# Kernel tuning notes

Measured on AMD Instinct MI355X. Metric: run time of the kernel, lower is better.

The kernel has to match this reference:

```python
import jax, jax.numpy as jnp
import numpy as np

B, F, M, D = 1024, 4, 512, 8192  # batch, factors, codebook size, hypervector dim
ITERS = 10


def _sign(x):
    # bipolar quantize: >=0 -> +1, <0 -> -1 (MAP VSA 'multiset quantize' / sign)
    return jnp.where(x >= 0, 1.0, -1.0).astype(x.dtype)


def setup_inputs() -> dict:
    key = jax.random.key(0)
    k1, k2 = jax.random.split(key, 2)
    # bipolar codebooks: (F, M, D)
    codebooks = _sign(jax.random.normal(k1, (F, M, D), dtype=jnp.float32))
    # composite input: bind (elementwise product) of one random codevector per factor
    idx = jax.random.randint(k2, (B, F), 0, M)  # ground-truth factor indices
    chosen = codebooks[jnp.arange(F)[None, :], idx]  # (B, F, D)
    inp = jnp.prod(chosen, axis=1)  # (B, D), bipolar
    # init estimates = quantized multiset (superposition) of each codebook, per the
    # module's get_init_estimates, broadcast over batch
    init_est = jnp.broadcast_to(_sign(codebooks.sum(axis=1))[None], (B, F, D))
    init_est = jnp.asarray(init_est, dtype=jnp.float32)
    return {"input": inp, "init_estimates": init_est, "codebooks": codebooks}


def reference(input, init_estimates, codebooks):
    """CONCURRENT resonator, SOFTWARE (bipolar MAP) mode, activation='NONE'.

    Returns (outcome indices (B,F) int32, convergence iteration k, final estimates).
    """

    def stage(est):
        # For bipolar +/-1 vectors: multibind(all other factors) = prod(all) * est
        prod_all = jnp.prod(est, axis=1)                      # (B, D)
        new_est = input[:, None, :] * prod_all[:, None, :] * est  # (B, F, D)
        sim = jnp.einsum('bfd,fmd->bfm', new_est, codebooks)  # dot_similarity
        out = _sign(jnp.einsum('bfm,fmd->bfd', sim, codebooks))  # multiset, quantize
        return out, sim.max(axis=-1)

    def step(carry, _):
        est, k, done = carry
        new_est, _max_sim = stage(est)
        conv = jnp.all(new_est == est)  # old_estimates == estimates check
        k = k + jnp.where(done, 0, 1)
        done = done | conv
        return (new_est, k, done), None

    init = (init_estimates, jnp.array(0, jnp.int32), jnp.array(False))
    (est, k, _done), _ = jax.lax.scan(step, init, None, length=ITERS)

    # cleanup: argmax of |dot_similarity| per factor (argmax_abs=True)
    sim = jnp.einsum('bfd,fmd->bfm', est, codebooks)
    outcome = jnp.argmax(jnp.abs(sim), axis=-1).astype(jnp.int32)  # (B, F)
    return outcome, k, est
```

## Files before the change

### kernel.cpp

```cpp
#include <hip/hip_runtime.h>
#include <stdint.h>

#define B_ 1024
#define F_ 4
#define M_ 512
#define D_ 8192
#define ITERS_ 10
#define DW_ 128
#define SMSZ2 32768

typedef unsigned long long u64;
typedef unsigned int u32;
typedef unsigned short u16;
typedef signed char i8;

typedef int i32x4 __attribute__((ext_vector_type(4)));
typedef u64 u64x2 __attribute__((ext_vector_type(2)));

struct Flags { u32 done; u32 k; u32 conv[ITERS_]; };

__device__ inline void gload_lds16(const void* g, void* l){
  __builtin_amdgcn_global_load_lds(
      (const __attribute__((address_space(1))) void*)g,
      (__attribute__((address_space(3))) void*)l, 16, 0, 0);
}

__device__ inline bool conv_prefix_done(const u32* conv, int iter){
  bool d = false;
  for (int j = 0; j < iter; ++j) d |= (conv[j] != 0u);
  return d;
}

__global__ void k_bitify(const float* __restrict__ src, u64* __restrict__ dst){
  long gid = (long)blockIdx.x * 256 + threadIdx.x;
  float v = src[gid];
  u64 m = __ballot(v < 0.0f);
  if ((threadIdx.x & 63) == 0) dst[gid >> 6] = m;
}

__global__ void k_bitify0(const float* __restrict__ init_est, u64* __restrict__ tmp0,
                          Flags* fl){
  long gid = (long)blockIdx.x * 256 + threadIdx.x;
  float v = init_est[gid];
  u64 m = __ballot(v < 0.0f);
  if ((threadIdx.x & 63) == 0) tmp0[gid >> 6] = m;
  if (blockIdx.x == 0){
    if (threadIdx.x == 0){ fl->done = 0; fl->k = 0; }
    if (threadIdx.x < ITERS_) fl->conv[threadIdx.x] = 1u;
  }
}

__global__ void k_bcast(const u64* __restrict__ tmp0, u64* __restrict__ estbits){
  long gid = (long)blockIdx.x * 256 + threadIdx.x;
  estbits[gid] = tmp0[gid & (F_*DW_ - 1)];
}

__global__ void k_cb_prep(const float* __restrict__ cb, u64* __restrict__ cbbT,
                          i8* __restrict__ cbT8){
  __shared__ i8 tile[64][68];
  int bx = blockIdx.x;
  int f = bx >> 10;
  int r = bx & 1023;
  int mt = r >> 7, dt = r & 127;
  for (int it = 0; it < 16; ++it){
    int lid = threadIdx.x + it*256;
    int i = lid >> 6, j = lid & 63;
    float v = cb[((long)(f*M_ + mt*64 + i))*D_ + dt*64 + j];
    tile[j][i] = (v < 0.0f) ? (i8)-1 : (i8)1;
    u64 msk = __ballot(v < 0.0f);
    if (j == 0) cbbT[((long)(f*DW_ + dt))*M_ + mt*64 + i] = msk;
  }
  __syncthreads();
  for (int it = 0; it < 4; ++it){
    int lid = threadIdx.x + it*256;
    int dd = lid >> 4, mg = lid & 15;
    u32 p = (u32)(unsigned char)tile[dd][mg*4+0]
          | ((u32)(unsigned char)tile[dd][mg*4+1] << 8)
          | ((u32)(unsigned char)tile[dd][mg*4+2] << 16)
          | ((u32)(unsigned char)tile[dd][mg*4+3] << 24);
    *(u32*)(cbT8 + ((long)(f*D_ + dt*64 + dd))*M_ + mt*64 + mg*4) = p;
  }
}

__global__ __launch_bounds__(256) void k_forward2(
    const u64* __restrict__ inbits, const u64* __restrict__ estbits,
    const u64* __restrict__ cbbT, i8* __restrict__ Aq, i8* __restrict__ Ar,
    const Flags* __restrict__ fl, int iter){
  if (conv_prefix_done(fl->conv, iter)) return;
  __shared__ u64 nbs[DW_][10];
  int id = blockIdx.x;
  int rr = id & 7;
  int f   = rr & 3;
  int btl = rr >> 2;
  int q   = id >> 3;
  int bth = q & 63;
  int mh  = q >> 6;
  int bt  = bth*2 + btl;
  int b0  = bt * 8;
  int tid = threadIdx.x;
  for (int idx = tid; idx < 8*DW_; idx += 256){
    int w = idx & 127, bb = idx >> 7;
    const u64* eb = estbits + (long)(b0 + bb)*F_*DW_;
    u64 all = eb[w] ^ eb[DW_+w] ^ eb[2*DW_+w] ^ eb[3*DW_+w];
    nbs[w][bb] = inbits[(long)(b0 + bb)*DW_ + w] ^ all ^ eb[f*DW_ + w];
  }
  __syncthreads();
  int m = mh*256 + tid;
  int acc[8];
  #pragma unroll
  for (int bb = 0; bb < 8; ++bb) acc[bb] = 0;
  const u64* cbf = cbbT + (long)f*DW_*M_ + m;
  #pragma unroll 2
  for (int w = 0; w < DW_; ++w){
    u64 c = cbf[(long)w*M_];
    u64x2 n01 = *(const u64x2*)&nbs[w][0];
    u64x2 n23 = *(const u64x2*)&nbs[w][2];
    u64x2 n45 = *(const u64x2*)&nbs[w][4];
    u64x2 n67 = *(const u64x2*)&nbs[w][6];
    acc[0] += (int)__popcll(n01.x ^ c);
    acc[1] += (int)__popcll(n01.y ^ c);
    acc[2] += (int)__popcll(n23.x ^ c);
    acc[3] += (int)__popcll(n23.y ^ c);
    acc[4] += (int)__popcll(n45.x ^ c);
    acc[5] += (int)__popcll(n45.y ^ c);
    acc[6] += (int)__popcll(n67.x ^ c);
    acc[7] += (int)__popcll(n67.y ^ c);
  }
  #pragma unroll
  for (int bb = 0; bb < 8; ++bb){
    int v = 4096 - acc[bb];
    int r = ((v + 32) & 63) - 32;
    int qd = (v - r) >> 6;
    long base = ((long)(f*B_ + b0 + bb))*M_ + m;
    Aq[base] = (i8)qd;
    Ar[base] = (i8)r;
  }
}

__global__ __launch_bounds__(256, 2) void k_backward_d256(
    const i8* __restrict__ Aq, const i8* __restrict__ Ar, const i8* __restrict__ cbT8,
    u64* __restrict__ estbits, Flags* fl, int iter){
  if (conv_prefix_done(fl->conv, iter)) return;
  __shared__ __attribute__((aligned(16))) i8 smem[2*SMSZ2];
  int id = blockIdx.x;
  int rr = id & 7;
  int f  = rr >> 1;
  int dh = rr & 1;
  int qq = id >> 3;
  int bt = qq & 7;
  int dtl= qq >> 3;
  int dtp= dh*16 + dtl;
  int b0 = bt*128, d0 = dtp*256;
  int tid = threadIdx.x;
  int wv = tid >> 6, lane = tid & 63, l16 = lane & 15, quad = lane >> 4;
  int rl = lane >> 2, pl = lane & 3;

  i32x4 zero = {0, 0, 0, 0};
  i32x4 acc[2][16];
  #pragma unroll
  for (int i = 0; i < 2; ++i)
    #pragma unroll
    for (int j = 0; j < 16; ++j) acc[i][j] = zero;

  const i8* Aqg = Aq + ((long)f*B_ + b0)*M_;
  const i8* Arg = Ar + ((long)f*B_ + b0)*M_;
  const i8* Bg  = cbT8 + ((long)f*D_ + d0)*M_;

  const i8* gsrc[8];
  i8* lbase[8];
  int swz = (rl >> 1) & 3;
  #pragma unroll
  for (int j2 = 0; j2 < 8; ++j2){
    int job = j2*4 + wv;
    const i8* src; i8* lb; int jj;
    if (job < 8)      { src = Aqg; jj = job;      lb = smem +         jj*1024; }
    else if (job < 16){ src = Arg; jj = job - 8;  lb = smem +  8192 + jj*1024; }
    else              { src = Bg;  jj = job - 16; lb = smem + 16384 + jj*1024; }
    gsrc[j2]  = src + (long)(jj*16 + rl)*M_ + ((pl ^ swz) << 4);
    lbase[j2] = lb;
  }

  #pragma unroll
  for (int j2 = 0; j2 < 8; ++j2)
    gload_lds16(gsrc[j2], lbase[j2]);

  for (int kt = 0; kt < 8; ++kt){
    __syncthreads();
    if (kt < 7){
      int nb = (kt + 1) & 1, k0 = (kt + 1)*64;
      #pragma unroll
      for (int j2 = 0; j2 < 8; ++j2)
        gload_lds16(gsrc[j2] + k0, lbase[j2] + nb*SMSZ2);
    }
    const i8* sb = smem + (kt & 1)*SMSZ2;
    i32x4 aq[2], ar[2];
    #pragma unroll
    for (int rt = 0; rt < 2; ++rt){
      int row = wv*32 + rt*16 + l16;
      int c = (quad ^ ((row >> 1) & 3)) << 4;
      aq[rt] = *(const i32x4*)(sb +        row*64 + c);
      ar[rt] = *(const i32x4*)(sb + 8192 + row*64 + c);
    }
    #pragma unroll
    for (int ct = 0; ct < 16; ++ct){
      int rowB = ct*16 + l16;
      int c = (quad ^ ((rowB >> 1) & 3)) << 4;
      i32x4 bb = *(const i32x4*)(sb + 16384 + rowB*64 + c);
      i32x4 bb64;
      #pragma unroll
      for (int g = 0; g < 4; ++g)
        bb64[g] = (int)(((u32)bb[g] << 6) & 0xC0C0C0C0u);
      acc[0][ct] = __builtin_amdgcn_mfma_i32_16x16x64_i8(aq[0], bb64, acc[0][ct], 0, 0, 0);
      acc[0][ct] = __builtin_amdgcn_mfma_i32_16x16x64_i8(ar[0], bb,   acc[0][ct], 0, 0, 0);
      acc[1][ct] = __builtin_amdgcn_mfma_i32_16x16x64_i8(aq[1], bb64, acc[1][ct], 0, 0, 0);
      acc[1][ct] = __builtin_amdgcn_mfma_i32_16x16x64_i8(ar[1], bb,   acc[1][ct], 0, 0, 0);
    }
  }

  int q3 = (lane >> 2) & 3, pw = lane & 3;
  int pw1 = pw & 1, pw2 = pw >> 1;
  u64 wreg[2][4];
  #pragma unroll
  for (int rt = 0; rt < 2; ++rt){
    #pragma unroll
    for (int r = 0; r < 4; ++r){
      u64 g0[4], g1[4], g2[4], g3[4];
      #pragma unroll
      for (int c = 0; c < 4; ++c){
        g0[c] = __ballot(acc[rt][c][r]      < 0);
        g1[c] = __ballot(acc[rt][4 + c][r]  < 0);
        g2[c] = __ballot(acc[rt][8 + c][r]  < 0);
        g3[c] = __ballot(acc[rt][12 + c][r] < 0);
      }
      u64 word = 0;
      #pragma unroll
      for (int c = 0; c < 4; ++c){
        u64 s = pw2 ? (pw1 ? g3[c] : g2[c]) : (pw1 ? g1[c] : g0[c]);
        word |= ((s >> (16*q3)) & 0xFFFFull) << (16*c);
      }
      wreg[rt][r] = word;
    }
  }
  u64 oldv[2][4];
  if (lane < 16){
    #pragma unroll
    for (int rt = 0; rt < 2; ++rt)
      #pragma unroll
      for (int r = 0; r < 4; ++r){
        int row = wv*32 + rt*16 + q3*4 + r;
        oldv[rt][r] = estbits[((long)(b0 + row)*F_ + f)*DW_ + dtp*4 + pw];
      }
  }
  u32 flag = 0;
  if (lane < 16){
    #pragma unroll
    for (int rt = 0; rt < 2; ++rt)
      #pragma unroll
      for (int r = 0; r < 4; ++r){
        int row = wv*32 + rt*16 + q3*4 + r;
        long addr = ((long)(b0 + row)*F_ + f)*DW_ + dtp*4 + pw;
        estbits[addr] = wreg[rt][r];
        flag |= (oldv[rt][r] != wreg[rt][r]) ? 1u : 0u;
      }
  }
  u32 mymiss = (u32)(__ballot(flag != 0) != 0ull);
  if (lane == 0 && mymiss) atomicAnd(&fl->conv[iter], 0u);
}

__global__ __launch_bounds__(256) void k_outcome(
    const u64* __restrict__ estbits, const u64* __restrict__ cbbT,
    const Flags* __restrict__ fl, float* __restrict__ out){
  __shared__ u64 es[8][DW_];
  __shared__ int redv[4][8], redi[4][8];
  int f = blockIdx.y, b0 = blockIdx.x * 8;
  int tid = threadIdx.x, wv = tid >> 6, lane = tid & 63;
  for (int idx = tid; idx < 8*DW_; idx += 256){
    int bb = idx >> 7, w = idx & 127;
    es[bb][w] = estbits[((long)(b0 + bb)*F_ + f)*DW_ + w];
  }
  __syncthreads();
  const u64* cbf = cbbT + (long)f*DW_*M_;
  int m0 = tid, m1 = tid + 256;
  int acc0[8], acc1[8];
  #pragma unroll
  for (int bb = 0; bb < 8; ++bb){ acc0[bb] = 0; acc1[bb] = 0; }
  for (int w = 0; w < DW_; ++w){
    u64 c0 = cbf[(long)w*M_ + m0];
    u64 c1 = cbf[(long)w*M_ + m1];
    #pragma unroll
    for (int bb = 0; bb < 8; ++bb){
      u64 e = es[bb][w];
      acc0[bb] += (int)__popcll(e ^ c0);
      acc1[bb] += (int)__popcll(e ^ c1);
    }
  }
  int bv[8], bi[8];
  #pragma unroll
  for (int bb = 0; bb < 8; ++bb){
    int a0 = 4096 - acc0[bb]; if (a0 < 0) a0 = -a0;
    int a1 = 4096 - acc1[bb]; if (a1 < 0) a1 = -a1;
    bv[bb] = a0; bi[bb] = m0;
    if (a1 > a0){ bv[bb] = a1; bi[bb] = m1; }
  }
  for (int off = 32; off; off >>= 1){
    #pragma unroll
    for (int bb = 0; bb < 8; ++bb){
      int ov = __shfl_xor(bv[bb], off, 64);
      int oi = __shfl_xor(bi[bb], off, 64);
      if (ov > bv[bb] || (ov == bv[bb] && oi < bi[bb])){ bv[bb] = ov; bi[bb] = oi; }
    }
  }
  if (lane == 0)
    #pragma unroll
    for (int bb = 0; bb < 8; ++bb){ redv[wv][bb] = bv[bb]; redi[wv][bb] = bi[bb]; }
  __syncthreads();
  if (tid < 8){
    int v0 = redv[0][tid], i0 = redi[0][tid];
    for (int w = 1; w < 4; ++w){
      int v = redv[w][tid], i = redi[w][tid];
      if (v > v0 || (v == v0 && i < i0)){ v0 = v; i0 = i; }
    }
    out[(long)(b0 + tid)*F_ + f] = (float)i0;
  }
  if (blockIdx.x == 0 && f == 0 && tid == 0){
    int k = ITERS_;
    for (int j = 0; j < ITERS_; ++j) if (fl->conv[j]){ k = j + 1; break; }
    out[B_*F_] = (float)k;
  }
}

__global__ void k_unpack(const u64* __restrict__ estbits, float* __restrict__ out){
  long gid = (long)blockIdx.x*256 + threadIdx.x;
  int bf = (int)(gid >> 11);
  int d4 = (int)(gid & 2047);
  u64 word = estbits[(long)bf*DW_ + (d4 >> 4)];
  u32 nib = (u32)(word >> ((d4 & 15) * 4)) & 0xFu;
  long base = (long)(B_*F_ + 1) + (long)bf*D_ + (long)d4*4;
  out[base+0] = (nib & 1u) ? -1.0f : 1.0f;
  out[base+1] = (nib & 2u) ? -1.0f : 1.0f;
  out[base+2] = (nib & 4u) ? -1.0f : 1.0f;
  out[base+3] = (nib & 8u) ? -1.0f : 1.0f;
}

extern "C" void kernel_launch(void* const* d_in, const int* in_sizes, int n_in,
                              void* d_out, int out_size, void* d_ws, size_t ws_size,
                              hipStream_t stream){
  const float* input    = (const float*)d_in[0];
  const float* init_est = (const float*)d_in[1];
  const float* cb       = (const float*)d_in[2];
  char* ws   = (char*)d_ws;
  char* outc = (char*)d_out;

  size_t off = 0;
  Flags* fl = (Flags*)(ws); off = 1024;
  u64* tmp0    = (u64*)(ws + off); off += (size_t)F_*DW_*8;
  off = (off + 1023) & ~size_t(1023);
  u64* inbits  = (u64*)(ws + off); off += (size_t)B_*DW_*8;
  u64* estbits = (u64*)(ws + off); off += (size_t)B_*F_*DW_*8;
  u64* cbbT    = (u64*)(ws + off); off += (size_t)F_*DW_*M_*8;
  size_t big = (size_t)F_*D_*M_ + 2*(size_t)F_*B_*M_;
  i8 *cbT8, *Aq, *Ar;
  if (ws_size >= off + big + 1024){
    cbT8 = (i8*)(ws + off); off += (size_t)F_*D_*M_;
    Aq   = (i8*)(ws + off); off += (size_t)F_*B_*M_;
    Ar   = (i8*)(ws + off); off += (size_t)F_*B_*M_;
  } else {
    cbT8 = (i8*)(outc + (80ull << 20));
    Aq   = (i8*)(outc + (100ull << 20));
    Ar   = (i8*)(outc + (104ull << 20));
  }

  k_bitify0<<<(F_*D_)/256, 256, 0, stream>>>(init_est, tmp0, fl);
  k_bcast<<<(B_*F_*DW_)/256, 256, 0, stream>>>(tmp0, estbits);
  k_bitify<<<(B_*(long)D_)/256, 256, 0, stream>>>(input, inbits);
  k_cb_prep<<<4096, 256, 0, stream>>>(cb, cbbT, cbT8);

  for (int it = 0; it < ITERS_; ++it){
    k_forward2<<<1024, 256, 0, stream>>>(inbits, estbits, cbbT, Aq, Ar, fl, it);
    k_backward_d256<<<1024, 256, 0, stream>>>(Aq, Ar, cbT8, estbits, fl, it);
  }

  k_outcome<<<dim3(B_/8, F_), 256, 0, stream>>>(estbits, cbbT, fl, (float*)d_out);
  k_unpack<<<((long)B_*F_*D_/4)/256, 256, 0, stream>>>(estbits, (float*)d_out);
}
```

Measured before the change: 1.395 ms.

## Widen backward tile to 512 columns with 8 waves and triple-buffered LDS

The backward GEMM block now covers 128 batch rows by 512 D columns with 512 threads (8 waves split 4x2), which halves the grid and lets one A tile (Aq/Ar) in LDS serve twice as many codebook columns. The K loop moves from double to triple buffering in dynamic shared memory, with explicit vmcnt waits and raw barriers so loads run two stages ahead. The cost is 144KB of LDS per block, which likely allows only one block per CU, and a heavier reliance on hand-written wait counts for correctness.

```diff
diff --git a/kernel.cpp b/kernel.cpp
--- a/kernel.cpp
+++ b/kernel.cpp
@@ -7,7 +7,7 @@
 #define D_ 8192
 #define ITERS_ 10
 #define DW_ 128
-#define SMSZ2 32768
+#define BUFSZ 49152
 
 typedef unsigned long long u64;
 typedef unsigned int u32;
@@ -137,11 +137,11 @@
   }
 }
 
-__global__ __launch_bounds__(256, 2) void k_backward_d256(
+__global__ __launch_bounds__(512, 2) void k_backward_d512(
     const i8* __restrict__ Aq, const i8* __restrict__ Ar, const i8* __restrict__ cbT8,
     u64* __restrict__ estbits, Flags* fl, int iter){
   if (conv_prefix_done(fl->conv, iter)) return;
-  __shared__ __attribute__((aligned(16))) i8 smem[2*SMSZ2];
+  extern __shared__ __attribute__((aligned(16))) i8 smem[];
   int id = blockIdx.x;
   int rr = id & 7;
   int f  = rr >> 1;
@@ -149,10 +149,11 @@
   int qq = id >> 3;
   int bt = qq & 7;
   int dtl= qq >> 3;
-  int dtp= dh*16 + dtl;
-  int b0 = bt*128, d0 = dtp*256;
+  int dtp= dh*8 + dtl;
+  int b0 = bt*128, d0 = dtp*512;
   int tid = threadIdx.x;
   int wv = tid >> 6, lane = tid & 63, l16 = lane & 15, quad = lane >> 4;
+  int wr = wv & 3, wc = wv >> 2;
   int rl = lane >> 2, pl = lane & 3;
 
   i32x4 zero = {0, 0, 0, 0};
@@ -166,56 +167,63 @@
   const i8* Arg = Ar + ((long)f*B_ + b0)*M_;
   const i8* Bg  = cbT8 + ((long)f*D_ + d0)*M_;
 
-  const i8* gsrc[8];
-  i8* lbase[8];
   int swz = (rl >> 1) & 3;
-  #pragma unroll
-  for (int j2 = 0; j2 < 8; ++j2){
-    int job = j2*4 + wv;
-    const i8* src; i8* lb; int jj;
-    if (job < 8)      { src = Aqg; jj = job;      lb = smem +         jj*1024; }
-    else if (job < 16){ src = Arg; jj = job - 8;  lb = smem +  8192 + jj*1024; }
-    else              { src = Bg;  jj = job - 16; lb = smem + 16384 + jj*1024; }
+  const i8* gsrc[6]; int lbase[6];
+  #pragma unroll
+  for (int j2 = 0; j2 < 6; ++j2){
+    int job = j2*8 + wv;
+    const i8* src; int lb; int jj;
+    if (job < 8)      { src = Aqg; jj = job;      lb =         jj*1024; }
+    else if (job < 16){ src = Arg; jj = job - 8;  lb =  8192 + jj*1024; }
+    else              { src = Bg;  jj = job - 16; lb = 16384 + jj*1024; }
     gsrc[j2]  = src + (long)(jj*16 + rl)*M_ + ((pl ^ swz) << 4);
     lbase[j2] = lb;
   }
 
-  #pragma unroll
-  for (int j2 = 0; j2 < 8; ++j2)
-    gload_lds16(gsrc[j2], lbase[j2]);
-
+#define ISSUE_KT(KT) do{ \
+    i8* ba_ = smem + ((KT) % 3) * BUFSZ; const int k0_ = (KT)*64; \
+    _Pragma("unroll") \
+    for (int j2_ = 0; j2_ < 6; ++j2_) \
+      gload_lds16(gsrc[j2_] + k0_, ba_ + lbase[j2_]); \
+  }while(0)
+
+  ISSUE_KT(0);
+  ISSUE_KT(1);
+
+  #pragma unroll
   for (int kt = 0; kt < 8; ++kt){
-    __syncthreads();
-    if (kt < 7){
-      int nb = (kt + 1) & 1, k0 = (kt + 1)*64;
-      #pragma unroll
-      for (int j2 = 0; j2 < 8; ++j2)
-        gload_lds16(gsrc[j2] + k0, lbase[j2] + nb*SMSZ2);
-    }
-    const i8* sb = smem + (kt & 1)*SMSZ2;
+    if (kt < 7) asm volatile("s_waitcnt vmcnt(6)" ::: "memory");
+    else        asm volatile("s_waitcnt vmcnt(0)" ::: "memory");
+    __builtin_amdgcn_s_barrier();
+    asm volatile("" ::: "memory");
+    __builtin_amdgcn_sched_barrier(0);
+    if (kt < 6) ISSUE_KT(kt + 2);
+
+    const i8* sb = smem + (kt % 3) * BUFSZ;
     i32x4 aq[2], ar[2];
     #pragma unroll
     for (int rt = 0; rt < 2; ++rt){
-      int row = wv*32 + rt*16 + l16;
+      int row = wr*32 + rt*16 + l16;
       int c = (quad ^ ((row >> 1) & 3)) << 4;
       aq[rt] = *(const i32x4*)(sb +        row*64 + c);
       ar[rt] = *(const i32x4*)(sb + 8192 + row*64 + c);
     }
     #pragma unroll
-    for (int ct = 0; ct < 16; ++ct){
-      int rowB = ct*16 + l16;
+    for (int ctl = 0; ctl < 16; ++ctl){
+      int rowB = wc*256 + ctl*16 + l16;
       int c = (quad ^ ((rowB >> 1) & 3)) << 4;
       i32x4 bb = *(const i32x4*)(sb + 16384 + rowB*64 + c);
       i32x4 bb64;
       #pragma unroll
       for (int g = 0; g < 4; ++g)
         bb64[g] = (int)(((u32)bb[g] << 6) & 0xC0C0C0C0u);
-      acc[0][ct] = __builtin_amdgcn_mfma_i32_16x16x64_i8(aq[0], bb64, acc[0][ct], 0, 0, 0);
-      acc[0][ct] = __builtin_amdgcn_mfma_i32_16x16x64_i8(ar[0], bb,   acc[0][ct], 0, 0, 0);
-      acc[1][ct] = __builtin_amdgcn_mfma_i32_16x16x64_i8(aq[1], bb64, acc[1][ct], 0, 0, 0);
-      acc[1][ct] = __builtin_amdgcn_mfma_i32_16x16x64_i8(ar[1], bb,   acc[1][ct], 0, 0, 0);
-    }
-  }
+      acc[0][ctl] = __builtin_amdgcn_mfma_i32_16x16x64_i8(aq[0], bb64, acc[0][ctl], 0, 0, 0);
+      acc[0][ctl] = __builtin_amdgcn_mfma_i32_16x16x64_i8(ar[0], bb,   acc[0][ctl], 0, 0, 0);
+      acc[1][ctl] = __builtin_amdgcn_mfma_i32_16x16x64_i8(aq[1], bb64, acc[1][ctl], 0, 0, 0);
+      acc[1][ctl] = __builtin_amdgcn_mfma_i32_16x16x64_i8(ar[1], bb,   acc[1][ctl], 0, 0, 0);
+    }
+  }
+#undef ISSUE_KT
 
   int q3 = (lane >> 2) & 3, pw = lane & 3;
   int pw1 = pw & 1, pw2 = pw >> 1;
@@ -247,8 +255,8 @@
     for (int rt = 0; rt < 2; ++rt)
       #pragma unroll
       for (int r = 0; r < 4; ++r){
-        int row = wv*32 + rt*16 + q3*4 + r;
-        oldv[rt][r] = estbits[((long)(b0 + row)*F_ + f)*DW_ + dtp*4 + pw];
+        int row = wr*32 + rt*16 + q3*4 + r;
+        oldv[rt][r] = estbits[((long)(b0 + row)*F_ + f)*DW_ + dtp*8 + wc*4 + pw];
       }
   }
   u32 flag = 0;
@@ -257,8 +265,8 @@
     for (int rt = 0; rt < 2; ++rt)
       #pragma unroll
       for (int r = 0; r < 4; ++r){
-        int row = wv*32 + rt*16 + q3*4 + r;
-        long addr = ((long)(b0 + row)*F_ + f)*DW_ + dtp*4 + pw;
+        int row = wr*32 + rt*16 + q3*4 + r;
+        long addr = ((long)(b0 + row)*F_ + f)*DW_ + dtp*8 + wc*4 + pw;
         estbits[addr] = wreg[rt][r];
         flag |= (oldv[rt][r] != wreg[rt][r]) ? 1u : 0u;
       }
@@ -350,6 +358,13 @@
   const float* cb       = (const float*)d_in[2];
   char* ws   = (char*)d_ws;
   char* outc = (char*)d_out;
+
+  static int s_attr = 0;
+  if (!s_attr){
+    hipFuncSetAttribute((const void*)k_backward_d512,
+                        hipFuncAttributeMaxDynamicSharedMemorySize, 3*BUFSZ);
+    s_attr = 1;
+  }
 
   size_t off = 0;
   Flags* fl = (Flags*)(ws); off = 1024;
@@ -377,7 +392,7 @@
 
   for (int it = 0; it < ITERS_; ++it){
     k_forward2<<<1024, 256, 0, stream>>>(inbits, estbits, cbbT, Aq, Ar, fl, it);
-    k_backward_d256<<<1024, 256, 0, stream>>>(Aq, Ar, cbT8, estbits, fl, it);
+    k_backward_d512<<<512, 512, 3*BUFSZ, stream>>>(Aq, Ar, cbT8, estbits, fl, it);
   }
 
   k_outcome<<<dim3(B_/8, F_), 256, 0, stream>>>(estbits, cbbT, fl, (float*)d_out);
```

Measured after the change: 1.470 ms, median of 2. 5.4% more time.

## Triple-buffer codebook tiles in backward GEMM with split A/B prefetch

Applied to the files above, without the earlier changes.

Restructures the backward int8 MFMA kernel's LDS pipeline. A tiles stay double-buffered, while codebook B tiles are now triple-buffered and prefetched two k-steps ahead. Explicit vmcnt waits and raw barriers replace __syncthreads, so one stage of loads can remain in flight across the barrier. Shared memory grows to 80 KB of dynamic LDS, which could limit the two-blocks-per-CU occupancy the launch bounds target.

```diff
diff --git a/kernel.cpp b/kernel.cpp
--- a/kernel.cpp
+++ b/kernel.cpp
@@ -7,7 +7,6 @@
 #define D_ 8192
 #define ITERS_ 10
 #define DW_ 128
-#define SMSZ2 32768
 
 typedef unsigned long long u64;
 typedef unsigned int u32;
@@ -137,11 +136,11 @@
   }
 }
 
-__global__ __launch_bounds__(256, 2) void k_backward_d256(
+__global__ __launch_bounds__(256, 2) void k_backward_d256r(
     const i8* __restrict__ Aq, const i8* __restrict__ Ar, const i8* __restrict__ cbT8,
     u64* __restrict__ estbits, Flags* fl, int iter){
   if (conv_prefix_done(fl->conv, iter)) return;
-  __shared__ __attribute__((aligned(16))) i8 smem[2*SMSZ2];
+  extern __shared__ __attribute__((aligned(16))) i8 smem[];
   int id = blockIdx.x;
   int rr = id & 7;
   int f  = rr >> 1;
@@ -166,46 +165,59 @@
   const i8* Arg = Ar + ((long)f*B_ + b0)*M_;
   const i8* Bg  = cbT8 + ((long)f*D_ + d0)*M_;
 
-  const i8* gsrc[8];
-  i8* lbase[8];
   int swz = (rl >> 1) & 3;
-  #pragma unroll
-  for (int j2 = 0; j2 < 8; ++j2){
+  const i8* gA[4]; int lA[4]; const i8* gB[4]; int lB[4];
+  #pragma unroll
+  for (int j2 = 0; j2 < 4; ++j2){
     int job = j2*4 + wv;
-    const i8* src; i8* lb; int jj;
-    if (job < 8)      { src = Aqg; jj = job;      lb = smem +         jj*1024; }
-    else if (job < 16){ src = Arg; jj = job - 8;  lb = smem +  8192 + jj*1024; }
-    else              { src = Bg;  jj = job - 16; lb = smem + 16384 + jj*1024; }
-    gsrc[j2]  = src + (long)(jj*16 + rl)*M_ + ((pl ^ swz) << 4);
-    lbase[j2] = lb;
-  }
-
-  #pragma unroll
-  for (int j2 = 0; j2 < 8; ++j2)
-    gload_lds16(gsrc[j2], lbase[j2]);
-
+    const i8* srcA = (job < 8) ? Aqg : Arg;
+    int jj = job & 7;
+    gA[j2] = srcA + (long)(jj*16 + rl)*M_ + ((pl ^ swz) << 4);
+    lA[j2] = ((job < 8) ? 0 : 8192) + jj*1024;
+    gB[j2] = Bg + (long)(job*16 + rl)*M_ + ((pl ^ swz) << 4);
+    lB[j2] = job*1024;
+  }
+
+#define ISSUE_A(KT) do{ \
+    i8* ba_ = smem + ((KT)&1)*16384; const int k0_ = (KT)*64; \
+    _Pragma("unroll") \
+    for (int j_ = 0; j_ < 4; ++j_) gload_lds16(gA[j_] + k0_, ba_ + lA[j_]); \
+  }while(0)
+#define ISSUE_B(KT) do{ \
+    i8* bb_ = smem + 32768 + ((KT)%3)*16384; const int k0_ = (KT)*64; \
+    _Pragma("unroll") \
+    for (int j_ = 0; j_ < 4; ++j_) gload_lds16(gB[j_] + k0_, bb_ + lB[j_]); \
+  }while(0)
+
+  ISSUE_A(0);
+  ISSUE_B(0);
+  ISSUE_B(1);
+
+  #pragma unroll
   for (int kt = 0; kt < 8; ++kt){
-    __syncthreads();
-    if (kt < 7){
-      int nb = (kt + 1) & 1, k0 = (kt + 1)*64;
-      #pragma unroll
-      for (int j2 = 0; j2 < 8; ++j2)
-        gload_lds16(gsrc[j2] + k0, lbase[j2] + nb*SMSZ2);
-    }
-    const i8* sb = smem + (kt & 1)*SMSZ2;
+    if (kt < 7) asm volatile("s_waitcnt vmcnt(4)" ::: "memory");
+    else        asm volatile("s_waitcnt vmcnt(0)" ::: "memory");
+    __builtin_amdgcn_s_barrier();
+    asm volatile("" ::: "memory");
+    __builtin_amdgcn_sched_barrier(0);
+    if (kt + 1 < 8) ISSUE_A(kt + 1);
+    if (kt + 2 < 8) ISSUE_B(kt + 2);
+
+    const i8* sa  = smem + (kt & 1)*16384;
+    const i8* sbB = smem + 32768 + (kt % 3)*16384;
     i32x4 aq[2], ar[2];
     #pragma unroll
     for (int rt = 0; rt < 2; ++rt){
       int row = wv*32 + rt*16 + l16;
       int c = (quad ^ ((row >> 1) & 3)) << 4;
-      aq[rt] = *(const i32x4*)(sb +        row*64 + c);
-      ar[rt] = *(const i32x4*)(sb + 8192 + row*64 + c);
+      aq[rt] = *(const i32x4*)(sa +        row*64 + c);
+      ar[rt] = *(const i32x4*)(sa + 8192 + row*64 + c);
     }
     #pragma unroll
     for (int ct = 0; ct < 16; ++ct){
       int rowB = ct*16 + l16;
       int c = (quad ^ ((rowB >> 1) & 3)) << 4;
-      i32x4 bb = *(const i32x4*)(sb + 16384 + rowB*64 + c);
+      i32x4 bb = *(const i32x4*)(sbB + rowB*64 + c);
       i32x4 bb64;
       #pragma unroll
       for (int g = 0; g < 4; ++g)
@@ -216,6 +228,8 @@
       acc[1][ct] = __builtin_amdgcn_mfma_i32_16x16x64_i8(ar[1], bb,   acc[1][ct], 0, 0, 0);
     }
   }
+#undef ISSUE_A
+#undef ISSUE_B
 
   int q3 = (lane >> 2) & 3, pw = lane & 3;
   int pw1 = pw & 1, pw2 = pw >> 1;
@@ -350,6 +364,13 @@
   const float* cb       = (const float*)d_in[2];
   char* ws   = (char*)d_ws;
   char* outc = (char*)d_out;
+
+  static int s_attr = 0;
+  if (!s_attr){
+    hipFuncSetAttribute((const void*)k_backward_d256r,
+                        hipFuncAttributeMaxDynamicSharedMemorySize, 81920);
+    s_attr = 1;
+  }
 
   size_t off = 0;
   Flags* fl = (Flags*)(ws); off = 1024;
@@ -377,7 +398,7 @@
 
   for (int it = 0; it < ITERS_; ++it){
     k_forward2<<<1024, 256, 0, stream>>>(inbits, estbits, cbbT, Aq, Ar, fl, it);
-    k_backward_d256<<<1024, 256, 0, stream>>>(Aq, Ar, cbT8, estbits, fl, it);
+    k_backward_d256r<<<1024, 256, 81920, stream>>>(Aq, Ar, cbT8, estbits, fl, it);
   }
 
   k_outcome<<<dim3(B_/8, F_), 256, 0, stream>>>(estbits, cbbT, fl, (float*)d_out);
```

Result: no change. 1.396 ms (+0.1%).
